# Optimization experiments

Hardware: AMD Instinct MI355X
Metric: run time of the kernel (lower is better)

The kernel has to match this reference:

```python
import jax, jax.numpy as jnp
import numpy as np

# Dimensions (see shape_source):
B = 256    # number of nodes (atoms)
C = 64     # num_features (channels)
Y = 16     # spherical basis size: dims of 0e+1o+2e+3o = 1+3+5+7
Z = 23     # number of symmetric-contraction paths (U.size(-1))
E = 10     # n_node_attributes (number of chemical elements, one-hot)
CORR = 3   # correlation order -> spare dims 'wxv'
CG_DENSITY = 0.1  # CG coefficient tensors are highly sparse


def setup_inputs() -> dict:
    key = jax.random.key(0)
    kU, kM, kW, kZ, kA = jax.random.split(key, 5)
    # U buffer: shape (Y,)*CORR + (Y, Z) = (16,16,16,16,23), sparse like real CG coeffs
    U = jax.random.normal(kU, (Y,) * CORR + (Y, Z), dtype=jnp.float32)
    mask = jax.random.uniform(kM, U.shape) < CG_DENSITY
    U = U * mask.astype(jnp.float32)
    # W parameter: (n_node_attributes, Z, num_features), init randn/Z as in module
    W = jax.random.normal(kW, (E, Z, C), dtype=jnp.float32) / Z
    # node embeddings: (B, C, Y)  ('bci' in the einsum)
    node_embeddings = jax.random.normal(kZ, (B, C, Y), dtype=jnp.float32)
    # node attributes: one-hot element encodings (B, E)  ('be')
    elem = jax.random.randint(kA, (B,), 0, E)
    node_attributes = jax.nn.one_hot(elem, E, dtype=jnp.float32)
    return {
        "U": U,
        "W": W,
        "node_embeddings": node_embeddings,
        "node_attributes": node_attributes,
    }


def reference(U, W, node_embeddings, node_attributes):
    # Faithful to: torch.einsum('wxvik,ekc,bci,be->bcwxv', U, W, z, a)
    # Efficient contraction order (avoids any (B,*,Y^3) intermediate except the output):
    Wb = jnp.einsum('ekc,be->bkc', W, node_attributes)        # (B, Z, C): per-node path weights
    P = jnp.einsum('bkc,bci->bcik', Wb, node_embeddings)      # (B, C, Y, Z)
    out = jnp.einsum('wxvik,bcik->bcwxv', U, P)               # (B, C, Y, Y, Y)
    return out
```

## Files before the change

### kernel.cpp

```cpp
#include <hip/hip_runtime.h>
#include <hip/hip_bf16.h>

#define B_NODES 256
#define C_FEAT  64
#define Y_DIM   16
#define Z_PATH  23
#define E_ATTR  10
#define WXV     4096
#define K_REAL  368
#define K_PAD   384
#define M_DIM   16384
#define N_DIM   4096
#define GRP_STRIDE 6144
#define W_STRIDE   512

typedef __attribute__((ext_vector_type(8))) short bf16x8;
typedef __attribute__((ext_vector_type(8))) unsigned short u16x8;
typedef __attribute__((ext_vector_type(4))) float f32x4;

__device__ inline unsigned short f2bf(float x) {
    union { float f; unsigned u; } v; v.f = x;
    unsigned r = v.u + 0x7fffu + ((v.u >> 16) & 1u);
    return (unsigned short)(r >> 16);
}

__device__ inline void gload_lds16(const void* g, void* l) {
    __builtin_amdgcn_global_load_lds(
        (const __attribute__((address_space(1))) void*)g,
        (__attribute__((address_space(3))) void*)l,
        16, 0, 0);
}

__global__ __launch_bounds__(256) void prep_combined(
    const float* __restrict__ U, const float* __restrict__ W,
    const float* __restrict__ z, const float* __restrict__ attr,
    unsigned short* __restrict__ At, unsigned short* __restrict__ Bt)
{
    int blk = blockIdx.x;
    int tid = threadIdx.x;
    if (blk < B_NODES) {
        int b = blk;
        __shared__ float t_lds[Z_PATH * C_FEAT];
        __shared__ float z_lds[C_FEAT * Y_DIM];
        __shared__ float a_lds[E_ATTR];
        if (tid < E_ATTR) a_lds[tid] = attr[b * E_ATTR + tid];
        ((float4*)z_lds)[tid] = ((const float4*)(z + (size_t)b * 1024))[tid];
        __syncthreads();
        for (int idx = tid; idx < Z_PATH * C_FEAT; idx += 256) {
            int k = idx >> 6;
            int c = idx & 63;
            float acc = 0.f;
            #pragma unroll
            for (int e = 0; e < E_ATTR; ++e)
                acc += a_lds[e] * W[(e * Z_PATH + k) * C_FEAT + c];
            t_lds[idx] = acc;
        }
        __syncthreads();
        for (int u = tid; u < C_FEAT * 48; u += 256) {
            int c = u / 48;
            int g = u - c * 48;
            int j0 = g * 8;
            u16x8 pack;
            #pragma unroll
            for (int jj = 0; jj < 8; ++jj) {
                int j = j0 + jj;
                float v = 0.f;
                if (j < K_REAL) {
                    int i = j / Z_PATH;
                    int k = j - i * Z_PATH;
                    v = z_lds[c * Y_DIM + i] * t_lds[k * C_FEAT + c];
                }
                pack[jj] = f2bf(v);
            }
            int rg = b * 4 + (c >> 4);
            size_t off = (size_t)rg * GRP_STRIDE + (g >> 2) * W_STRIDE
                       + ((g & 3) * 16 + (c & 15)) * 8;
            *(u16x8*)&At[off] = pack;
        }
    } else {
        int f = (blk - B_NODES) * 256 + tid;
        int row = f / 48;
        int g = f - row * 48;
        int j0 = g * 8;
        u16x8 pack;
        #pragma unroll
        for (int jj = 0; jj < 8; ++jj) {
            int j = j0 + jj;
            pack[jj] = (j < K_REAL) ? f2bf(U[(size_t)row * K_REAL + j]) : (unsigned short)0;
        }
        size_t off = (size_t)(row >> 4) * GRP_STRIDE + (g >> 2) * W_STRIDE
                   + ((g & 3) * 16 + (row & 15)) * 8;
        *(u16x8*)&Bt[off] = pack;
    }
}

__global__ __launch_bounds__(512, 4) void gemm_kernel(
    const unsigned short* __restrict__ At,
    const unsigned short* __restrict__ Bt,
    float* __restrict__ C)
{
    __shared__ __align__(16) unsigned short sB[4 * GRP_STRIDE];

    int bid = blockIdx.x;
    int wg = (bid & 7) * 512 + (bid >> 3);
    int tm = wg >> 6;
    int tn = wg & 63;
    int tid = threadIdx.x;
    int lane = tid & 63;
    int ww = tid >> 6;

    const char* gB = (const char*)(Bt + (size_t)tn * 4 * GRP_STRIDE);
    #pragma unroll
    for (int i = 0; i < 6; ++i) {
        int chunk = ww * 6 + i;
        gload_lds16(gB + chunk * 1024 + lane * 16, (char*)sB + chunk * 1024);
    }

    const unsigned short* pA = At + (size_t)(tm * 16 + ww * 2) * GRP_STRIDE + lane * 8;

    bf16x8 af[12][2];
    bf16x8 bf[12][4];

    #pragma unroll
    for (int f = 0; f < 2; ++f) {
        af[0][f] = *(const bf16x8*)(pA + f * GRP_STRIDE + 0 * W_STRIDE);
        af[1][f] = *(const bf16x8*)(pA + f * GRP_STRIDE + 1 * W_STRIDE);
    }

    __syncthreads();

    const char* sBb = (const char*)sB + (size_t)lane * 16;
    #pragma unroll
    for (int g = 0; g < 4; ++g)
        bf[0][g] = *(const bf16x8*)(sBb + (size_t)(g * GRP_STRIDE + 0 * W_STRIDE) * 2);

    f32x4 acc[2][4];
    #pragma unroll
    for (int p = 0; p < 2; ++p)
        #pragma unroll
        for (int q = 0; q < 4; ++q)
            acc[p][q] = (f32x4){0.f, 0.f, 0.f, 0.f};

    #pragma unroll
    for (int w = 0; w < 12; ++w) {
        if (w + 2 < 12) {
            #pragma unroll
            for (int f = 0; f < 2; ++f)
                af[w + 2][f] = *(const bf16x8*)(pA + f * GRP_STRIDE + (w + 2) * W_STRIDE);
        }
        if (w + 1 < 12) {
            #pragma unroll
            for (int g = 0; g < 4; ++g)
                bf[w + 1][g] = *(const bf16x8*)(sBb + (size_t)(g * GRP_STRIDE + (w + 1) * W_STRIDE) * 2);
        }
        #pragma unroll
        for (int fm = 0; fm < 2; ++fm)
            #pragma unroll
            for (int fn = 0; fn < 4; ++fn)
                acc[fm][fn] = __builtin_amdgcn_mfma_f32_16x16x32_bf16(
                    af[w][fm], bf[w][fn], acc[fm][fn], 0, 0, 0);
    }

    int r0 = tm * 256 + ww * 32 + (lane >> 4) * 4;
    int c0 = tn * 64 + (lane & 15);
    #pragma unroll
    for (int fm = 0; fm < 2; ++fm)
        #pragma unroll
        for (int reg = 0; reg < 4; ++reg)
            #pragma unroll
            for (int fn = 0; fn < 4; ++fn)
                __builtin_nontemporal_store(acc[fm][fn][reg],
                    &C[(size_t)(r0 + fm * 16 + reg) * N_DIM + (c0 + fn * 16)]);
}

__global__ __launch_bounds__(256) void fallback_kernel(
    const float* __restrict__ U, const float* __restrict__ W,
    const float* __restrict__ z, const float* __restrict__ attr,
    float* __restrict__ out)
{
    int bc = blockIdx.x;
    int b = bc >> 6, c = bc & 63;
    int tid = threadIdx.x;
    __shared__ float zt[K_REAL];
    for (int idx = tid; idx < K_REAL; idx += 256) {
        int i = idx / Z_PATH;
        int k = idx - i * Z_PATH;
        float t = 0.f;
        #pragma unroll
        for (int e = 0; e < E_ATTR; ++e)
            t += attr[b * E_ATTR + e] * W[(e * Z_PATH + k) * C_FEAT + c];
        zt[idx] = z[((size_t)b * C_FEAT + c) * Y_DIM + i] * t;
    }
    __syncthreads();
    for (int n = tid; n < WXV; n += 256) {
        const float* Ur = U + (size_t)n * K_REAL;
        float s = 0.f;
        for (int j = 0; j < K_REAL; ++j) s += Ur[j] * zt[j];
        out[(size_t)bc * WXV + n] = s;
    }
}

extern "C" void kernel_launch(void* const* d_in, const int* in_sizes, int n_in,
                              void* d_out, int out_size, void* d_ws, size_t ws_size,
                              hipStream_t stream)
{
    const float* U    = (const float*)d_in[0];
    const float* W    = (const float*)d_in[1];
    const float* z    = (const float*)d_in[2];
    const float* attr = (const float*)d_in[3];
    float* out = (float*)d_out;

    size_t needA = (size_t)M_DIM * K_PAD * sizeof(unsigned short);
    size_t needU = (size_t)N_DIM * K_PAD * sizeof(unsigned short);
    if (ws_size >= needA + needU) {
        unsigned short* At = (unsigned short*)d_ws;
        unsigned short* Bt = At + (size_t)M_DIM * K_PAD;
        prep_combined<<<B_NODES + (N_DIM * 48) / 256, 256, 0, stream>>>(U, W, z, attr, At, Bt);
        gemm_kernel<<<4096, 512, 0, stream>>>(At, Bt, out);
    } else {
        fallback_kernel<<<M_DIM, 256, 0, stream>>>(U, W, z, attr, out);
    }
}
```

Before: 91.04 us.

## Make GEMM blocks persistent over four M sub-tiles, reusing LDS-resident B tile

Each GEMM workgroup now handles four consecutive 256-row M tiles for the same N tile, so the B tile is loaded into LDS once and reused four times. The grid shrinks from 4096 to 1024 blocks, and the A fragments for the next sub-tile are prefetched during the tail of the current sub-tile's K loop. This cuts redundant B global-to-LDS traffic and per-block launch/sync overhead. The cost is less parallelism, fewer blocks to hide store latency, and higher register pressure from the prefetch buffers.

Measured after the change: 114.0 us. +25.2%, slower.

```diff
diff --git a/kernel.cpp b/kernel.cpp
--- a/kernel.cpp
+++ b/kernel.cpp
@@ -102,8 +102,8 @@
     __shared__ __align__(16) unsigned short sB[4 * GRP_STRIDE];
 
     int bid = blockIdx.x;
-    int wg = (bid & 7) * 512 + (bid >> 3);
-    int tm = wg >> 6;
+    int wg = (bid & 7) * 128 + (bid >> 3);
+    int tmg = wg >> 6;
     int tn = wg & 63;
     int tid = threadIdx.x;
     int lane = tid & 63;
@@ -116,61 +116,82 @@
         gload_lds16(gB + chunk * 1024 + lane * 16, (char*)sB + chunk * 1024);
     }
 
-    const unsigned short* pA = At + (size_t)(tm * 16 + ww * 2) * GRP_STRIDE + lane * 8;
-
-    bf16x8 af[12][2];
-    bf16x8 bf[12][4];
-
+    const unsigned short* pA0 =
+        At + (size_t)(tmg * 64 + ww * 2) * GRP_STRIDE + lane * 8;
+
+    bf16x8 afn[4][2];
     #pragma unroll
-    for (int f = 0; f < 2; ++f) {
-        af[0][f] = *(const bf16x8*)(pA + f * GRP_STRIDE + 0 * W_STRIDE);
-        af[1][f] = *(const bf16x8*)(pA + f * GRP_STRIDE + 1 * W_STRIDE);
-    }
+    for (int v = 0; v < 4; ++v)
+        #pragma unroll
+        for (int f = 0; f < 2; ++f)
+            afn[v][f] = *(const bf16x8*)(pA0 + f * GRP_STRIDE + v * W_STRIDE);
 
     __syncthreads();
 
     const char* sBb = (const char*)sB + (size_t)lane * 16;
+
     #pragma unroll
-    for (int g = 0; g < 4; ++g)
-        bf[0][g] = *(const bf16x8*)(sBb + (size_t)(g * GRP_STRIDE + 0 * W_STRIDE) * 2);
-
-    f32x4 acc[2][4];
-    #pragma unroll
-    for (int p = 0; p < 2; ++p)
-        #pragma unroll
-        for (int q = 0; q < 4; ++q)
-            acc[p][q] = (f32x4){0.f, 0.f, 0.f, 0.f};
-
-    #pragma unroll
-    for (int w = 0; w < 12; ++w) {
-        if (w + 2 < 12) {
+    for (int sub = 0; sub < 4; ++sub) {
+        const unsigned short* pAc = pA0 + (size_t)(sub * 16) * GRP_STRIDE;
+        const unsigned short* pAn = pA0 + (size_t)((sub + 1) * 16) * GRP_STRIDE;
+        const char* sBp = sBb;
+        asm volatile("" : "+v"(sBp));
+
+        bf16x8 af[12][2];
+        #pragma unroll
+        for (int v = 0; v < 4; ++v)
             #pragma unroll
             for (int f = 0; f < 2; ++f)
-                af[w + 2][f] = *(const bf16x8*)(pA + f * GRP_STRIDE + (w + 2) * W_STRIDE);
-        }
-        if (w + 1 < 12) {
-            #pragma unroll
-            for (int g = 0; g < 4; ++g)
-                bf[w + 1][g] = *(const bf16x8*)(sBb + (size_t)(g * GRP_STRIDE + (w + 1) * W_STRIDE) * 2);
-        }
+                af[v][f] = afn[v][f];
+
+        bf16x8 bq[12][4];
+        #pragma unroll
+        for (int g = 0; g < 4; ++g)
+            bq[0][g] = *(const bf16x8*)(sBp + (size_t)(g * GRP_STRIDE) * 2);
+
+        f32x4 acc[2][4];
+        #pragma unroll
+        for (int p = 0; p < 2; ++p)
+            #pragma unroll
+            for (int q = 0; q < 4; ++q)
+                acc[p][q] = (f32x4){0.f, 0.f, 0.f, 0.f};
+
+        #pragma unroll
+        for (int w = 0; w < 12; ++w) {
+            if (w >= 2 && w <= 9) {
+                #pragma unroll
+                for (int f = 0; f < 2; ++f)
+                    af[w + 2][f] = *(const bf16x8*)(pAc + f * GRP_STRIDE + (w + 2) * W_STRIDE);
+            }
+            if (w >= 8 && sub < 3) {
+                #pragma unroll
+                for (int f = 0; f < 2; ++f)
+                    afn[w - 8][f] = *(const bf16x8*)(pAn + f * GRP_STRIDE + (w - 8) * W_STRIDE);
+            }
+            if (w < 11) {
+                #pragma unroll
+                for (int g = 0; g < 4; ++g)
+                    bq[w + 1][g] = *(const bf16x8*)(sBp + (size_t)(g * GRP_STRIDE + (w + 1) * W_STRIDE) * 2);
+            }
+            #pragma unroll
+            for (int fm = 0; fm < 2; ++fm)
+                #pragma unroll
+                for (int fn = 0; fn < 4; ++fn)
+                    acc[fm][fn] = __builtin_amdgcn_mfma_f32_16x16x32_bf16(
+                        af[w][fm], bq[w][fn], acc[fm][fn], 0, 0, 0);
+        }
+
+        int r0 = (tmg * 4 + sub) * 256 + ww * 32 + (lane >> 4) * 4;
+        int c0 = tn * 64 + (lane & 15);
         #pragma unroll
         for (int fm = 0; fm < 2; ++fm)
             #pragma unroll
-            for (int fn = 0; fn < 4; ++fn)
-                acc[fm][fn] = __builtin_amdgcn_mfma_f32_16x16x32_bf16(
-                    af[w][fm], bf[w][fn], acc[fm][fn], 0, 0, 0);
-    }
-
-    int r0 = tm * 256 + ww * 32 + (lane >> 4) * 4;
-    int c0 = tn * 64 + (lane & 15);
-    #pragma unroll
-    for (int fm = 0; fm < 2; ++fm)
-        #pragma unroll
-        for (int reg = 0; reg < 4; ++reg)
-            #pragma unroll
-            for (int fn = 0; fn < 4; ++fn)
-                __builtin_nontemporal_store(acc[fm][fn][reg],
-                    &C[(size_t)(r0 + fm * 16 + reg) * N_DIM + (c0 + fn * 16)]);
+            for (int reg = 0; reg < 4; ++reg)
+                #pragma unroll
+                for (int fn = 0; fn < 4; ++fn)
+                    __builtin_nontemporal_store(acc[fm][fn][reg],
+                        &C[(size_t)(r0 + fm * 16 + reg) * N_DIM + (c0 + fn * 16)]);
+    }
 }
 
 __global__ __launch_bounds__(256) void fallback_kernel(
@@ -216,7 +237,7 @@
         unsigned short* At = (unsigned short*)d_ws;
         unsigned short* Bt = At + (size_t)M_DIM * K_PAD;
         prep_combined<<<B_NODES + (N_DIM * 48) / 256, 256, 0, stream>>>(U, W, z, attr, At, Bt);
-        gemm_kernel<<<4096, 512, 0, stream>>>(At, Bt, out);
+        gemm_kernel<<<1024, 512, 0, stream>>>(At, Bt, out);
     } else {
         fallback_kernel<<<M_DIM, 256, 0, stream>>>(U, W, z, attr, out);
     }
```
